# Optimization experiments

Measured on AMD Instinct MI355X. Metric: run time of the kernel, lower is better.

The kernel has to match this reference:

```python
import jax, jax.numpy as jnp
import numpy as np
from math import sqrt

DIM = 2048
N_HEADS = 2
HEAD_DIM = DIM // N_HEADS  # 1024 == RoPE dims (dim // 2)
ROPE_DIMS = DIM // 2
ROPE_BASE = 10000.0


def apply_rope(x, dims=ROPE_DIMS, base=ROPE_BASE, offset=0):
    # x: [B, H, L, Dh]; non-traditional (split-half) RoPE over sequence axis
    L = x.shape[-2]
    pos = jnp.arange(offset, offset + L, dtype=x.dtype)[:, None]          # [L,1]
    inv = jnp.exp(jnp.arange(0, dims, 2, dtype=x.dtype) * (-np.log(base) / dims))  # [dims//2]
    theta = pos * inv                                                      # [L, dims//2]
    cos, sin = jnp.cos(theta), jnp.sin(theta)
    h = dims // 2
    x1, x2 = x[..., :h], x[..., h:dims]
    rx1 = x1 * cos - x2 * sin
    rx2 = x1 * sin + x2 * cos
    if dims < x.shape[-1]:
        return jnp.concatenate([rx1, rx2, x[..., dims:]], axis=-1)
    return jnp.concatenate([rx1, rx2], axis=-1)


def setup_inputs() -> dict:
    key = jax.random.key(0)
    ks = jax.random.split(key, 6)
    B, L = 4, 2048
    x = jax.random.normal(ks[0], (B, L, DIM), dtype=jnp.float32)
    # causal additive mask
    causal = jnp.tril(jnp.ones((L, L), dtype=bool))
    mask = jnp.where(causal, 0.0, -1e9).astype(jnp.float32)
    s1 = 1.0 / sqrt(DIM)
    Wqkv_w = jax.random.normal(ks[1], (3 * DIM, DIM), dtype=jnp.float32) * s1
    Wqkv_b = jnp.zeros((3 * DIM,), dtype=jnp.float32)
    out_w = jax.random.normal(ks[2], (DIM, DIM), dtype=jnp.float32) * s1
    out_b = jnp.zeros((DIM,), dtype=jnp.float32)
    return {"x": x, "mask": mask, "Wqkv_w": Wqkv_w, "Wqkv_b": Wqkv_b,
            "out_w": out_w, "out_b": out_b}


def reference(x, mask, Wqkv_w, Wqkv_b, out_w, out_b):
    B, L, D = x.shape
    H, Dh = N_HEADS, HEAD_DIM
    qkv = x @ Wqkv_w.T + Wqkv_b                       # [B, L, 3D]
    q, k, v = jnp.split(qkv, 3, axis=-1)
    # b l (h d) -> b h l d
    split = lambda t: t.reshape(B, L, H, Dh).transpose(0, 2, 1, 3)
    q, k, v = split(q), split(k), split(v)
    q = apply_rope(q)
    k = apply_rope(k)
    scale = sqrt(1.0 / Dh)
    scores = jnp.einsum('bhld,bhkd->bhlk', q * scale, k)  # [B,H,L,L]
    scores = scores + mask                                 # additive causal mask
    probs = jax.nn.softmax(scores, axis=-1)
    vh = jnp.einsum('bhlk,bhkd->bhld', probs, v)
    vh = vh.transpose(0, 2, 1, 3).reshape(B, L, D)         # b h l d -> b l (h d)
    out = vh @ out_w.T + out_b
    return (out, k, v)
```

## Files before the change

### kernel.cpp

```cpp
#include <hip/hip_runtime.h>
#include <hip/hip_bf16.h>
#include <math.h>

typedef unsigned short u16;
typedef __attribute__((ext_vector_type(8))) __bf16 bf16x8;
typedef __attribute__((ext_vector_type(4))) float f32x4;

__device__ __forceinline__ u16 f2b(float f) {
  unsigned u = __builtin_bit_cast(unsigned, f);
  u += 0x7fffu + ((u >> 16) & 1u);
  return (u16)(u >> 16);
}
__device__ __forceinline__ float b2f(u16 h) {
  unsigned u = ((unsigned)h) << 16;
  return __builtin_bit_cast(float, u);
}

__device__ __forceinline__ void gld_lds16(const u16* g, u16* l) {
  __builtin_amdgcn_global_load_lds(
      (const __attribute__((address_space(1))) unsigned int*)g,
      (__attribute__((address_space(3))) unsigned int*)l, 16, 0, 0);
}

#define MFMA16(a, b, c) \
  c = __builtin_amdgcn_mfma_f32_16x16x32_bf16(a, b, c, 0, 0, 0)

template <class FC>
__device__ __forceinline__ void gemm128_body(const u16* A, int lda,
                                             const u16* B, int ldb, FC fc,
                                             int m0, int n0, int K) {
  __shared__ __align__(16) u16 As[128 * 64];
  __shared__ __align__(16) u16 Bs[128 * 64];
  const int tid = threadIdx.x;
  const int wave = tid >> 6;
  const int lane = tid & 63;
  const int srow = lane >> 3;
  const int scol = ((lane & 7) ^ srow) * 8;
  const int wm = (wave & 1) * 64;
  const int wn = (wave >> 1) * 64;
  const int fm = lane & 15;
  const int fs = fm & 7;

  const u16* Abase = A + (size_t)m0 * lda;
  const u16* Bbase = B + (size_t)n0 * ldb;
  const size_t aLane = (size_t)(wave * 8 + srow) * lda + scol;
  const size_t bLane = (size_t)(wave * 8 + srow) * ldb + scol;

  f32x4 acc[4][4];
#pragma unroll
  for (int i = 0; i < 4; ++i)
#pragma unroll
    for (int j = 0; j < 4; ++j) acc[i][j] = (f32x4){0.f, 0.f, 0.f, 0.f};

  for (int k0 = 0; k0 < K; k0 += 64) {
#pragma unroll
    for (int c = 0; c < 4; ++c) {
      gld_lds16(Abase + (aLane + (size_t)(c * 32) * lda + k0),
                &As[(c * 4 + wave) * 512]);
      gld_lds16(Bbase + (bLane + (size_t)(c * 32) * ldb + k0),
                &Bs[(c * 4 + wave) * 512]);
    }
    __syncthreads();
#pragma unroll
    for (int kk = 0; kk < 2; ++kk) {
      const int cb = kk * 4 + (lane >> 4);
      const int p8 = (cb ^ fs) * 8;
      bf16x8 af[4], bfr[4];
#pragma unroll
      for (int i = 0; i < 4; ++i)
        af[i] = *(const bf16x8*)&As[(wm + i * 16 + fm) * 64 + p8];
#pragma unroll
      for (int j = 0; j < 4; ++j)
        bfr[j] = *(const bf16x8*)&Bs[(wn + j * 16 + fm) * 64 + p8];
#pragma unroll
      for (int i = 0; i < 4; ++i)
#pragma unroll
        for (int j = 0; j < 4; ++j) MFMA16(af[i], bfr[j], acc[i][j]);
    }
    __syncthreads();
  }
  const int er = lane >> 4;
#pragma unroll
  for (int i = 0; i < 4; ++i)
#pragma unroll
    for (int j = 0; j < 4; ++j)
#pragma unroll
      for (int r = 0; r < 4; ++r) {
        int m = m0 + wm + i * 16 + er * 4 + r;
        int n = n0 + wn + j * 16 + fm;
        fc(m, n, acc[i][j][r]);
      }
}

template <class FC>
__device__ __forceinline__ void gemm256_body(const u16* A, int lda,
                                             const u16* B, int ldb, FC fc,
                                             int m0, int n0, int K) {
  __shared__ __align__(16) u16 As[2][16384];
  __shared__ __align__(16) u16 Bs[2][16384];
  const int tid = threadIdx.x;
  const int wave = tid >> 6;
  const int lane = tid & 63;
  const int wr = wave >> 2;
  const int wc = wave & 3;
  const int fm = lane & 15;
  const int cb4 = lane >> 4;
  const int fs = fm & 7;
  const int srow = lane >> 3;
  const int scol = ((lane & 7) ^ srow) * 8;

  const u16* Ab = A + (size_t)(m0 + srow) * lda + scol;
  const u16* Bb = B + (size_t)(n0 + srow) * ldb + scol;

  const int paRow = (wr * 128 + fm) * 64;
  const int pbRow = (wc * 64 + fm) * 64;
  const int q0 = (cb4 ^ fs) * 8;
  const int q1 = q0 ^ 32;

  f32x4 acc[8][4];
#pragma unroll
  for (int m = 0; m < 8; ++m)
#pragma unroll
    for (int n = 0; n < 4; ++n) acc[m][n] = (f32x4){0.f, 0.f, 0.f, 0.f};

  auto stA = [&](int bi, int h, int kg) {
    const u16* g = Ab + (size_t)(h * 128 + wave * 8) * lda + kg;
    gld_lds16(g, &As[bi][h * 8192 + wave * 512]);
    gld_lds16(g + (size_t)64 * lda, &As[bi][h * 8192 + (wave + 8) * 512]);
  };
  auto stB = [&](int bi, int h, int kg) {
    const u16* g = Bb + (size_t)(h * 128 + wave * 8) * ldb + kg;
    gld_lds16(g, &Bs[bi][h * 8192 + wave * 512]);
    gld_lds16(g + (size_t)64 * ldb, &Bs[bi][h * 8192 + (wave + 8) * 512]);
  };

  const int nkt = K >> 6;

  stB(0, 0, 0);
  stB(0, 1, 0);
  stA(0, 0, 0);
  stA(0, 1, 0);
  stB(1, 0, 64);
  stB(1, 1, 64);
  stA(1, 0, 64);
  asm volatile("s_waitcnt vmcnt(6)" ::: "memory");
  __builtin_amdgcn_s_barrier();

  int buf = 0;
  for (int T = 0; T < nkt; ++T, buf ^= 1) {
    const int kc = T * 64;
    const bool sA1 = (T + 1) < nkt;
    const bool sN2 = (T + 2) < nkt;
    bf16x8 af[8], bv[4][2];
#pragma unroll
    for (int m = 0; m < 8; ++m)
      af[m] = *(const bf16x8*)&As[buf][paRow + m * 1024 + q0];
#pragma unroll
    for (int n = 0; n < 4; ++n) {
      bv[n][0] = *(const bf16x8*)&Bs[buf][pbRow + n * 1024 + q0];
      bv[n][1] = *(const bf16x8*)&Bs[buf][pbRow + n * 1024 + q1];
    }
    if (sA1) stA(buf ^ 1, 1, kc + 64);
    __builtin_amdgcn_s_barrier();
    asm volatile("s_waitcnt lgkmcnt(0)" ::: "memory");
    __builtin_amdgcn_sched_barrier(0);
    __builtin_amdgcn_s_setprio(1);
#pragma unroll
    for (int m = 0; m < 8; ++m) {
      MFMA16(af[m], bv[0][0], acc[m][0]);
      MFMA16(af[m], bv[1][0], acc[m][1]);
    }
    __builtin_amdgcn_s_setprio(0);
    __builtin_amdgcn_s_barrier();
    if (sN2) stB(buf, 0, kc + 128);
    __builtin_amdgcn_s_barrier();
    __builtin_amdgcn_s_setprio(1);
#pragma unroll
    for (int m = 0; m < 8; ++m) {
      MFMA16(af[m], bv[2][0], acc[m][2]);
      MFMA16(af[m], bv[3][0], acc[m][3]);
    }
    __builtin_amdgcn_s_setprio(0);
    __builtin_amdgcn_s_barrier();
#pragma unroll
    for (int m = 0; m < 8; ++m)
      af[m] = *(const bf16x8*)&As[buf][paRow + m * 1024 + q1];
    if (sN2) stB(buf, 1, kc + 128);
    __builtin_amdgcn_s_barrier();
    asm volatile("s_waitcnt lgkmcnt(0)" ::: "memory");
    __builtin_amdgcn_sched_barrier(0);
    __builtin_amdgcn_s_setprio(1);
#pragma unroll
    for (int m = 0; m < 8; ++m) {
      MFMA16(af[m], bv[0][1], acc[m][0]);
      MFMA16(af[m], bv[1][1], acc[m][1]);
    }
    __builtin_amdgcn_s_setprio(0);
    __builtin_amdgcn_s_barrier();
    if (sN2) stA(buf, 0, kc + 128);
    __builtin_amdgcn_s_barrier();
    __builtin_amdgcn_s_setprio(1);
#pragma unroll
    for (int m = 0; m < 8; ++m) {
      MFMA16(af[m], bv[2][1], acc[m][2]);
      MFMA16(af[m], bv[3][1], acc[m][3]);
    }
    __builtin_amdgcn_s_setprio(0);
    if (sN2) {
      asm volatile("s_waitcnt vmcnt(6)" ::: "memory");
    } else if (sA1) {
      asm volatile("s_waitcnt vmcnt(0)" ::: "memory");
    }
    __builtin_amdgcn_s_barrier();
  }

  const int er = lane >> 4;
#pragma unroll
  for (int m = 0; m < 8; ++m)
#pragma unroll
    for (int n = 0; n < 4; ++n)
#pragma unroll
      for (int r = 0; r < 4; ++r)
        fc(m0 + wr * 128 + m * 16 + er * 4 + r, n0 + wc * 64 + n * 16 + fm,
           acc[m][n][r]);
}

struct EQKV {
  u16* qb;
  u16* kb;
  float* vout;
  const float* bias;
  __device__ __forceinline__ void operator()(int m, int n, float v) const {
    v += bias[n];
    int b = m >> 11, l = m & 2047;
    int part = n >> 11, nn = n & 2047, h = nn >> 10, d = nn & 1023;
    size_t idx = ((size_t)((b << 1) + h) * 2048 + l) * 1024 + d;
    if (part == 0)
      qb[idx] = f2b(v);
    else if (part == 1)
      kb[idx] = f2b(v);
    else
      vout[idx] = v;
  }
};
struct EScoreB {
  u16* S;
  __device__ __forceinline__ void operator()(int m, int n, float v) const {
    S[((size_t)m << 11) + n] = f2b(v * 0.03125f + (n > m ? -1.0e9f : 0.0f));
  }
};
struct EBf16 {
  u16* o;
  int ld;
  __device__ __forceinline__ void operator()(int m, int n, float v) const {
    o[(size_t)m * ld + n] = f2b(v);
  }
};
struct EOut {
  float* o;
  const float* bias;
  __device__ __forceinline__ void operator()(int m, int n, float v) const {
    o[((size_t)m << 11) + n] = v + bias[n];
  }
};

__device__ __forceinline__ u16* spz(u16* sp0, u16* sp1, int z) {
  return (z < 4) ? sp0 + (size_t)z * 4194304 : sp1 + (size_t)(z - 4) * 4194304;
}

__global__ void __launch_bounds__(256) k_cast3(const float* x, const float* w1,
                                               const float* w2, u16* xb,
                                               u16* w1b, u16* w2b) {
  long i = (long)(blockIdx.x * 256 + threadIdx.x) * 4;
  const float* src;
  u16* dst;
  long off;
  if (i < 16777216L) {
    src = x; dst = xb; off = i;
  } else if (i < 16777216L + 12582912L) {
    src = w1; dst = w1b; off = i - 16777216L;
  } else {
    src = w2; dst = w2b; off = i - 16777216L - 12582912L;
  }
  float4 f = *(const float4*)(src + off);
  ushort4 o;
  o.x = f2b(f.x);
  o.y = f2b(f.y);
  o.z = f2b(f.z);
  o.w = f2b(f.w);
  *(ushort4*)(dst + off) = o;
}

__global__ void __launch_bounds__(512, 2) k_qkv(const u16* xb, const u16* wb,
                                                const float* bias, u16* qb,
                                                u16* kb, float* vout) {
  gemm256_body(xb, 2048, wb, 2048, EQKV{qb, kb, vout, bias}, blockIdx.y * 256,
               blockIdx.x * 256, 2048);
}

__global__ void __launch_bounds__(256) k_rope(u16* qb, u16* kb, float* kout) {
  int l = blockIdx.x;
  int t = threadIdx.x;
  float lf = (float)l;
  const float c0 = (float)(-9.210340371976184 / 1024.0);
  float s0, c_0, s1, c_1;
  {
    float inv = __expf((float)(2 * t) * c0);
    __sincosf(lf * inv, &s0, &c_0);
    float inv2 = __expf((float)(2 * (t + 256)) * c0);
    __sincosf(lf * inv2, &s1, &c_1);
  }
#pragma unroll
  for (int bh = 0; bh < 8; ++bh) {
    size_t base = ((size_t)bh * 2048 + l) * 1024;
#pragma unroll
    for (int half = 0; half < 2; ++half) {
      int i = t + half * 256;
      float c = half ? c_1 : c_0;
      float s = half ? s1 : s0;
      float x1 = b2f(qb[base + i]), x2 = b2f(qb[base + 512 + i]);
      qb[base + i] = f2b(x1 * c - x2 * s);
      qb[base + 512 + i] = f2b(x1 * s + x2 * c);
      float y1 = b2f(kb[base + i]), y2 = b2f(kb[base + 512 + i]);
      float r1 = y1 * c - y2 * s, r2 = y1 * s + y2 * c;
      kb[base + i] = f2b(r1);
      kb[base + 512 + i] = f2b(r2);
      kout[base + i] = r1;
      kout[base + 512 + i] = r2;
    }
  }
}

__global__ void __launch_bounds__(256) k_transpose_v(const float* v, u16* vt) {
  __shared__ u16 tile[64][65];
  int bh = blockIdx.z;
  int d0 = blockIdx.x * 64, l0 = blockIdx.y * 64;
  const float* vb = v + (size_t)bh * 2048 * 1024;
  u16* vtb = vt + (size_t)bh * 1024 * 2048;
  int t = threadIdx.x;
  int c = t & 63, r4 = t >> 6;
#pragma unroll
  for (int r = 0; r < 16; ++r) {
    int row = r * 4 + r4;
    tile[row][c] = f2b(vb[(size_t)(l0 + row) * 1024 + d0 + c]);
  }
  __syncthreads();
#pragma unroll
  for (int r = 0; r < 16; ++r) {
    int drow = r * 4 + r4;
    vtb[(size_t)(d0 + drow) * 2048 + l0 + c] = tile[c][drow];
  }
}

__global__ void __launch_bounds__(256) k_score(const u16* qb, const u16* kb,
                                               u16* sp0, u16* sp1) {
  int m0 = blockIdx.y * 128, n0 = blockIdx.x * 128;
  if (n0 > m0) return;
  int z = blockIdx.z;
  const u16* q = qb + (size_t)z * 2048 * 1024;
  const u16* k = kb + (size_t)z * 2048 * 1024;
  gemm128_body(q, 1024, k, 1024, EScoreB{spz(sp0, sp1, z)}, m0, n0, 1024);
}

__global__ void __launch_bounds__(256) k_softmax(u16* sp0, u16* sp1) {
  int l = blockIdx.x, z = blockIdx.y;
  u16* row = spz(sp0, sp1, z) + ((size_t)l << 11);
  int t = threadIdx.x;
  int jend = ((l >> 8) + 1) << 8;
  __shared__ float red[4];
  float vals[8];
  float mx = -1e30f;
#pragma unroll
  for (int i = 0; i < 8; ++i) {
    int j = i * 256 + t;
    float v = (j <= l) ? b2f(row[j]) : -1e30f;
    vals[i] = v;
    mx = fmaxf(mx, v);
  }
#pragma unroll
  for (int off = 32; off; off >>= 1) mx = fmaxf(mx, __shfl_down(mx, off));
  if ((t & 63) == 0) red[t >> 6] = mx;
  __syncthreads();
  mx = fmaxf(fmaxf(red[0], red[1]), fmaxf(red[2], red[3]));
  __syncthreads();
  float sum = 0.f;
#pragma unroll
  for (int i = 0; i < 8; ++i) {
    int j = i * 256 + t;
    float e = (j <= l) ? __expf(vals[i] - mx) : 0.f;
    vals[i] = e;
    sum += e;
  }
#pragma unroll
  for (int off = 32; off; off >>= 1) sum += __shfl_down(sum, off);
  if ((t & 63) == 0) red[t >> 6] = sum;
  __syncthreads();
  sum = red[0] + red[1] + red[2] + red[3];
  float is = 1.0f / sum;
#pragma unroll
  for (int i = 0; i < 8; ++i) {
    int j = i * 256 + t;
    if (j < jend) row[j] = f2b(vals[i] * is);
  }
}

__global__ void __launch_bounds__(512, 2) k_pv(u16* sp0, u16* sp1,
                                               const u16* vt, u16* vh) {
  int z = blockIdx.z;
  int b = z >> 1, h = z & 1;
  int m0 = blockIdx.y * 256, n0 = blockIdx.x * 256;
  const u16* Pz = spz(sp0, sp1, z);
  const u16* vtb = vt + (size_t)z * 1024 * 2048;
  u16* outb = vh + (size_t)b * 2048 * 2048 + (size_t)h * 1024;
  int Keff = m0 + 256;
  gemm256_body(Pz, 2048, vtb, 2048, EBf16{outb, 2048}, m0, n0, Keff);
}

__global__ void __launch_bounds__(512, 2) k_out(const u16* vh, const u16* w2,
                                                const float* bias, float* out) {
  gemm256_body(vh, 2048, w2, 2048, EOut{out, bias}, blockIdx.y * 256,
               blockIdx.x * 256, 2048);
}

extern "C" void kernel_launch(void* const* d_in, const int* in_sizes, int n_in,
                              void* d_out, int out_size, void* d_ws,
                              size_t ws_size, hipStream_t stream) {
  const float* x = (const float*)d_in[0];
  const float* w1 = (const float*)d_in[2];
  const float* b1 = (const float*)d_in[3];
  const float* w2 = (const float*)d_in[4];
  const float* b2 = (const float*)d_in[5];
  float* out = (float*)d_out;
  float* kout = out + (size_t)16777216;
  float* vout = kout + (size_t)16777216;

  char* ws = (char*)d_ws;
  u16* xb = (u16*)ws;
  ws += (size_t)33554432;
  u16* w1b = (u16*)ws;
  ws += (size_t)25165824;
  u16* w2b = (u16*)ws;
  ws += (size_t)8388608;
  u16* qb = (u16*)ws;
  ws += (size_t)33554432;
  u16* kb = (u16*)ws;
  ws += (size_t)33554432;
  u16* vtb = (u16*)ws;
  ws += (size_t)33554432;
  u16* sp1 = (u16*)ws;
  u16* sp0 = xb;
  u16* vh = qb;

  k_cast3<<<32768, 256, 0, stream>>>(x, w1, w2, xb, w1b, w2b);
  k_qkv<<<dim3(24, 32), 512, 0, stream>>>(xb, w1b, b1, qb, kb, vout);
  k_rope<<<2048, 256, 0, stream>>>(qb, kb, kout);
  k_transpose_v<<<dim3(16, 32, 8), 256, 0, stream>>>(vout, vtb);
  k_score<<<dim3(16, 16, 8), 256, 0, stream>>>(qb, kb, sp0, sp1);
  k_softmax<<<dim3(2048, 8), 256, 0, stream>>>(sp0, sp1);
  k_pv<<<dim3(4, 8, 8), 512, 0, stream>>>(sp0, sp1, vtb, vh);
  k_out<<<dim3(8, 32), 512, 0, stream>>>(vh, w2b, b2, out);
}
```

Before: 807.8 us.

## Merge GEMM MFMA phases with interleaved LDS loads and XCD-aware tile remap

```diff
diff --git a/kernel.cpp b/kernel.cpp
--- a/kernel.cpp
+++ b/kernel.cpp
@@ -151,17 +151,16 @@
     const int kc = T * 64;
     const bool sA1 = (T + 1) < nkt;
     const bool sN2 = (T + 2) < nkt;
-    bf16x8 af[8], bv[4][2];
-#pragma unroll
-    for (int m = 0; m < 8; ++m)
-      af[m] = *(const bf16x8*)&As[buf][paRow + m * 1024 + q0];
+    bf16x8 af[8], bv[4][2], ag[8];
 #pragma unroll
     for (int n = 0; n < 4; ++n) {
       bv[n][0] = *(const bf16x8*)&Bs[buf][pbRow + n * 1024 + q0];
       bv[n][1] = *(const bf16x8*)&Bs[buf][pbRow + n * 1024 + q1];
     }
+#pragma unroll
+    for (int m = 0; m < 8; ++m)
+      af[m] = *(const bf16x8*)&As[buf][paRow + m * 1024 + q0];
     if (sA1) stA(buf ^ 1, 1, kc + 64);
-    __builtin_amdgcn_s_barrier();
     asm volatile("s_waitcnt lgkmcnt(0)" ::: "memory");
     __builtin_amdgcn_sched_barrier(0);
     __builtin_amdgcn_s_setprio(1);
@@ -169,44 +168,32 @@
     for (int m = 0; m < 8; ++m) {
       MFMA16(af[m], bv[0][0], acc[m][0]);
       MFMA16(af[m], bv[1][0], acc[m][1]);
+      MFMA16(af[m], bv[2][0], acc[m][2]);
+      MFMA16(af[m], bv[3][0], acc[m][3]);
+      ag[m] = *(const bf16x8*)&As[buf][paRow + m * 1024 + q1];
+      __builtin_amdgcn_sched_group_barrier(0x008, 4, 0);
+      __builtin_amdgcn_sched_group_barrier(0x100, 1, 0);
     }
     __builtin_amdgcn_s_setprio(0);
     __builtin_amdgcn_s_barrier();
-    if (sN2) stB(buf, 0, kc + 128);
-    __builtin_amdgcn_s_barrier();
-    __builtin_amdgcn_s_setprio(1);
-#pragma unroll
-    for (int m = 0; m < 8; ++m) {
-      MFMA16(af[m], bv[2][0], acc[m][2]);
-      MFMA16(af[m], bv[3][0], acc[m][3]);
-    }
-    __builtin_amdgcn_s_setprio(0);
-    __builtin_amdgcn_s_barrier();
-#pragma unroll
-    for (int m = 0; m < 8; ++m)
-      af[m] = *(const bf16x8*)&As[buf][paRow + m * 1024 + q1];
-    if (sN2) stB(buf, 1, kc + 128);
-    __builtin_amdgcn_s_barrier();
+    if (sN2) {
+      stB(buf, 0, kc + 128);
+      stB(buf, 1, kc + 128);
+    }
     asm volatile("s_waitcnt lgkmcnt(0)" ::: "memory");
     __builtin_amdgcn_sched_barrier(0);
     __builtin_amdgcn_s_setprio(1);
 #pragma unroll
     for (int m = 0; m < 8; ++m) {
-      MFMA16(af[m], bv[0][1], acc[m][0]);
-      MFMA16(af[m], bv[1][1], acc[m][1]);
+      MFMA16(ag[m], bv[0][1], acc[m][0]);
+      MFMA16(ag[m], bv[1][1], acc[m][1]);
+      MFMA16(ag[m], bv[2][1], acc[m][2]);
+      MFMA16(ag[m], bv[3][1], acc[m][3]);
     }
     __builtin_amdgcn_s_setprio(0);
     __builtin_amdgcn_s_barrier();
-    if (sN2) stA(buf, 0, kc + 128);
-    __builtin_amdgcn_s_barrier();
-    __builtin_amdgcn_s_setprio(1);
-#pragma unroll
-    for (int m = 0; m < 8; ++m) {
-      MFMA16(af[m], bv[2][1], acc[m][2]);
-      MFMA16(af[m], bv[3][1], acc[m][3]);
-    }
-    __builtin_amdgcn_s_setprio(0);
     if (sN2) {
+      stA(buf, 0, kc + 128);
       asm volatile("s_waitcnt vmcnt(6)" ::: "memory");
     } else if (sA1) {
       asm volatile("s_waitcnt vmcnt(0)" ::: "memory");
@@ -294,8 +281,12 @@
 __global__ void __launch_bounds__(512, 2) k_qkv(const u16* xb, const u16* wb,
                                                 const float* bias, u16* qb,
                                                 u16* kb, float* vout) {
-  gemm256_body(xb, 2048, wb, 2048, EQKV{qb, kb, vout, bias}, blockIdx.y * 256,
-               blockIdx.x * 256, 2048);
+  int wg = blockIdx.x;
+  int id2 = (wg & 7) * 96 + (wg >> 3);
+  int nt = id2 >> 5;
+  int mt = id2 & 31;
+  gemm256_body(xb, 2048, wb, 2048, EQKV{qb, kb, vout, bias}, mt * 256,
+               nt * 256, 2048);
 }
 
 __global__ void __launch_bounds__(256) k_rope(u16* qb, u16* kb, float* kout) {
@@ -418,8 +409,11 @@
 
 __global__ void __launch_bounds__(512, 2) k_out(const u16* vh, const u16* w2,
                                                 const float* bias, float* out) {
-  gemm256_body(vh, 2048, w2, 2048, EOut{out, bias}, blockIdx.y * 256,
-               blockIdx.x * 256, 2048);
+  int wg = blockIdx.x;
+  int id2 = (wg & 7) * 32 + (wg >> 3);
+  int nt = id2 >> 5;
+  int mt = id2 & 31;
+  gemm256_body(vh, 2048, w2, 2048, EOut{out, bias}, mt * 256, nt * 256, 2048);
 }
 
 extern "C" void kernel_launch(void* const* d_in, const int* in_sizes, int n_in,
@@ -452,11 +446,11 @@
   u16* vh = qb;
 
   k_cast3<<<32768, 256, 0, stream>>>(x, w1, w2, xb, w1b, w2b);
-  k_qkv<<<dim3(24, 32), 512, 0, stream>>>(xb, w1b, b1, qb, kb, vout);
+  k_qkv<<<768, 512, 0, stream>>>(xb, w1b, b1, qb, kb, vout);
   k_rope<<<2048, 256, 0, stream>>>(qb, kb, kout);
   k_transpose_v<<<dim3(16, 32, 8), 256, 0, stream>>>(vout, vtb);
   k_score<<<dim3(16, 16, 8), 256, 0, stream>>>(qb, kb, sp0, sp1);
   k_softmax<<<dim3(2048, 8), 256, 0, stream>>>(sp0, sp1);
   k_pv<<<dim3(4, 8, 8), 512, 0, stream>>>(sp0, sp1, vtb, vh);
-  k_out<<<dim3(8, 32), 512, 0, stream>>>(vh, w2b, b2, out);
-}
+  k_out<<<256, 512, 0, stream>>>(vh, w2b, b2, out);
+}
```

Result: no change. 807.7 us (-0.0%).
